# Kernel tuning notes

Hardware: AMD Instinct MI355X
Metric: run time of the kernel (lower is better)

## Reference

```python
import jax, jax.numpy as jnp
import numpy as np

NUM, B, C, H, W = 2, 8, 512, 32, 32


def setup_inputs() -> dict:
    key = jax.random.key(0)
    ks = jax.random.split(key, 6)
    s = 0.02  # weight init scale
    return {
        "feat_sources": jax.random.normal(ks[0], (NUM, B, C, H, W), jnp.float32),
        "feat_targets": jax.random.normal(ks[1], (NUM, B, C, H, W), jnp.float32),
        # 1x1 conv == per-pixel channel matmul: weight [num, C_out, C_in], bias [num, C]
        "Wq": jax.random.normal(ks[2], (NUM, C, C), jnp.float32) * s,
        "bq": jnp.zeros((NUM, C), jnp.float32),
        "Wk": jax.random.normal(ks[3], (NUM, C, C), jnp.float32) * s,
        "bk": jnp.zeros((NUM, C), jnp.float32),
        "Wv": jax.random.normal(ks[4], (NUM, C, C), jnp.float32) * s,
        "bv": jnp.zeros((NUM, C), jnp.float32),
    }


def reference(feat_sources, feat_targets, Wq, bq, Wk, bk, Wv, bv):
    num, Bt, Ct, Ht, Wt = feat_targets.shape
    HW = Ht * Wt
    tgt = feat_targets.reshape(num, Bt, Ct, HW)  # queries/values come from targets
    src = feat_sources.reshape(num, Bt, Ct, HW)  # keys come from sources

    # 1x1 conv projections (batched over the `num` heads of convs)
    Q = jnp.einsum('ioc,ibcn->ibno', Wq, tgt) + bq[:, None, None, :]   # (num, B, HW, C)
    K = jnp.einsum('joc,jbcn->jbon', Wk, src) + bk[:, None, :, None]   # (num, B, C, HW)
    V = jnp.einsum('ioc,ibcn->ibon', Wv, tgt) + bv[:, None, :, None]   # (num, B, C, HW)

    # energy[i, j] = bmm(pro_query_i, pro_key_j) over all target/source pairs
    energy = jnp.einsum('ibnc,jbcm->ijbnm', Q, K)                      # (num, num, B, HW, HW)

    # alpha: softmax over sources j of the scalar mean energy per (i, j)
    means = energy.mean(axis=(2, 3, 4))                                # (num, num)
    alphas = jax.nn.softmax(means, axis=1)

    # per-source softmax over keys, then summed across sources (torch.stack(...).sum(0))
    attn = jax.nn.softmax(energy, axis=-1).sum(axis=1)                 # (num, B, HW, HW)

    # out[b, c, n] = sum_m V[b, c, m] * attn[b, n, m]  (bmm(value, attention^T))
    out = jnp.einsum('ibcm,ibnm->ibcn', V, attn).reshape(num, Bt, Ct, Ht, Wt)
    return out, alphas
```

## Files before the change

### kernel.cpp

```cpp
#include <hip/hip_runtime.h>

#define NUMH 2
#define BATCH 8
#define CCH 512
#define HWN 1024

typedef unsigned short u16;
typedef unsigned int u32;
typedef _Float16 f16;
typedef __attribute__((ext_vector_type(8))) _Float16 f16x8;
typedef __attribute__((ext_vector_type(8))) short bf16x8;
typedef __attribute__((ext_vector_type(4))) float f32x4;

__device__ __forceinline__ u16 f2h(float x) {
    union { f16 h; u16 u; } cv;
    cv.h = (f16)x;
    return cv.u;
}
__device__ __forceinline__ u16 f2bf(float x) {
    u32 u = __float_as_uint(x);
    return (u16)((u + 0x7fffu + ((u >> 16) & 1u)) >> 16);
}
__device__ __forceinline__ float bf2f(u16 h) { return __uint_as_float(((u32)h) << 16); }

__device__ __forceinline__ float waveReduceSum(float v) {
#pragma unroll
    for (int off = 32; off > 0; off >>= 1) v += __shfl_xor(v, off);
    return v;
}

__global__ void zero_means_kernel(float* means) {
    if (threadIdx.x < 4) means[threadIdx.x] = 0.0f;
}
__global__ void zero_rs_kernel(float* rs, int n) {
    const int i = blockIdx.x * 256 + threadIdx.x;
    if (i < n) rs[i] = 0.0f;
}

__device__ __forceinline__ void stage_tile(const u16* __restrict__ src, int ld, int k0,
                                           u16* lds_arr, int w, int l) {
#pragma unroll
    for (int inst = 0; inst < 2; inst++) {
        const int p = w * 128 + inst * 64 + l;
        const int n = p >> 2;
        const int k4 = (p & 3) ^ ((n >> 1) & 3);
        const u16* g = src + n * ld + k0 + k4 * 8;
        u16* lp = lds_arr + (w * 128 + inst * 64) * 8;
        __builtin_amdgcn_global_load_lds(
            (const __attribute__((address_space(1))) u32*)g,
            (__attribute__((address_space(3))) u32*)lp, 16, 0, 0);
    }
}

template<bool BF>
__device__ __forceinline__ void mfma_block(const u16* sA, const u16* sB,
                                           int wr, int wc, int fr, int kq, f32x4 acc[4][4]) {
#define SLOT(row) (((row) * 4 + ((kq) ^ (((row) >> 1) & 3))) * 8)
    if constexpr (BF) {
        bf16x8 a[4], b[4];
#pragma unroll
        for (int mi = 0; mi < 4; mi++) a[mi] = *(const bf16x8*)(sA + SLOT(wr * 64 + mi * 16 + fr));
#pragma unroll
        for (int ni = 0; ni < 4; ni++) b[ni] = *(const bf16x8*)(sB + SLOT(wc * 64 + ni * 16 + fr));
#pragma unroll
        for (int mi = 0; mi < 4; mi++)
#pragma unroll
            for (int ni = 0; ni < 4; ni++)
                acc[mi][ni] = __builtin_amdgcn_mfma_f32_16x16x32_bf16(a[mi], b[ni], acc[mi][ni], 0, 0, 0);
    } else {
        f16x8 a[4], b[4];
#pragma unroll
        for (int mi = 0; mi < 4; mi++) a[mi] = *(const f16x8*)(sA + SLOT(wr * 64 + mi * 16 + fr));
#pragma unroll
        for (int ni = 0; ni < 4; ni++) b[ni] = *(const f16x8*)(sB + SLOT(wc * 64 + ni * 16 + fr));
#pragma unroll
        for (int mi = 0; mi < 4; mi++)
#pragma unroll
            for (int ni = 0; ni < 4; ni++)
                acc[mi][ni] = __builtin_amdgcn_mfma_f32_16x16x32_f16(a[mi], b[ni], acc[mi][ni], 0, 0, 0);
    }
#undef SLOT
}

template<bool BF>
__device__ __forceinline__ void mm_core(const u16* __restrict__ A, const u16* __restrict__ B,
                                        int K, int ldA, int ldB, u16* s, f32x4 acc[4][4]) {
    const int t = threadIdx.x, w = t >> 6, l = t & 63;
    const int wr = w >> 1, wc = w & 1, fr = l & 15, kq = l >> 4;
    u16 *sA0 = s, *sA1 = s + 4096, *sB0 = s + 8192, *sB1 = s + 12288;
    for (int k0 = 0; k0 < K; k0 += 64) {
        __syncthreads();
        stage_tile(A, ldA, k0, sA0, w, l);
        stage_tile(A, ldA, k0 + 32, sA1, w, l);
        stage_tile(B, ldB, k0, sB0, w, l);
        stage_tile(B, ldB, k0 + 32, sB1, w, l);
        __syncthreads();
        mfma_block<BF>(sA0, sB0, wr, wc, fr, kq, acc);
        mfma_block<BF>(sA1, sB1, wr, wc, fr, kq, acc);
    }
}

#define ACC_INIT(acc)                                         \
    f32x4 acc[4][4];                                          \
    _Pragma("unroll") for (int mi_ = 0; mi_ < 4; mi_++)       \
    _Pragma("unroll") for (int ni_ = 0; ni_ < 4; ni_++)       \
        acc[mi_][ni_] = (f32x4){0.f, 0.f, 0.f, 0.f};

#define SMEM_BYTES 33792

template<bool BF, bool BCOL, bool BROW>
__device__ __forceinline__ void epi_h16(char* smem, const f32x4 acc[4][4],
                                        const float* biasCol, const float* biasRow,
                                        u16* O, int ldO) {
    const int t = threadIdx.x, w = t >> 6, l = t & 63;
    const int wr = w >> 1, wc = w & 1, fr = l & 15, fq = l >> 4;
    u16* sb16 = (u16*)smem;
    u32* sb32 = (u32*)smem;
    __syncthreads();
#pragma unroll
    for (int ni = 0; ni < 4; ni++) {
        const int col = wc * 64 + ni * 16 + fr;
        const float bc = BCOL ? biasCol[col] : 0.0f;
#pragma unroll
        for (int mi = 0; mi < 4; mi++)
#pragma unroll
            for (int r = 0; r < 4; r++) {
                const int row = wr * 64 + mi * 16 + fq * 4 + r;
                const float v = acc[mi][ni][r] + bc + (BROW ? biasRow[row] : 0.0f);
                sb16[row * 132 + col] = BF ? f2bf(v) : f2h(v);
            }
    }
    __syncthreads();
#pragma unroll
    for (int it = 0; it < 8; it++) {
        const int idx = it * 256 + t;
        const int rr = idx >> 4, ch = idx & 15;
        const uint4 v4 = *(const uint4*)&sb32[rr * 66 + ch * 4];
        *(uint4*)&O[(size_t)rr * ldO + ch * 8] = v4;
    }
}

template<bool SCALE>
__device__ __forceinline__ void epi_f32(char* smem, const f32x4 acc[4][4],
                                        const float* ls, float* O, int ldO) {
    const int t = threadIdx.x, w = t >> 6, l = t & 63;
    const int wr = w >> 1, wc = w & 1, fr = l & 15, fq = l >> 4;
    float* sf = (float*)smem;
#pragma unroll
    for (int half = 0; half < 2; half++) {
        __syncthreads();
        if (wr == half) {
#pragma unroll
            for (int ni = 0; ni < 4; ni++) {
                const int col = wc * 64 + ni * 16 + fr;
                const float inv = SCALE ? 1.0f / ls[col] : 1.0f;
#pragma unroll
                for (int mi = 0; mi < 4; mi++)
#pragma unroll
                    for (int r = 0; r < 4; r++) {
                        const int rl = mi * 16 + fq * 4 + r;
                        sf[rl * 132 + col] = acc[mi][ni][r] * inv;
                    }
            }
        }
        __syncthreads();
#pragma unroll
        for (int it = 0; it < 8; it++) {
            const int idx = it * 256 + t;
            const int rr = idx >> 5, ch = idx & 31;
            const float4 v4 = *(const float4*)&sf[rr * 132 + ch * 4];
            *(float4*)&O[(size_t)(half * 64 + rr) * ldO + ch * 4] = v4;
        }
    }
}

__global__ __launch_bounds__(256) void tconv_kernel(
    const float* __restrict__ tgt, const float* __restrict__ src,
    u16* __restrict__ Tt, u16* __restrict__ St) {
    __shared__ float s[64][65];
    const int z = blockIdx.z;
    const int ib = z & 15;
    const float* X = (z >> 4 ? src : tgt) + (size_t)ib * CCH * HWN;
    u16* O = (z >> 4 ? St : Tt) + (size_t)ib * HWN * CCH;
    const int n0 = blockIdx.x * 64, c0 = blockIdx.y * 64;
    const int t = threadIdx.x;
    {
        const int cc = t >> 4, nch = (t & 15) * 4;
#pragma unroll
        for (int r = 0; r < 4; r++) {
            const float4 v = *(const float4*)&X[(size_t)(c0 + cc + r * 16) * HWN + n0 + nch];
            s[cc + r * 16][nch + 0] = v.x;
            s[cc + r * 16][nch + 1] = v.y;
            s[cc + r * 16][nch + 2] = v.z;
            s[cc + r * 16][nch + 3] = v.w;
        }
    }
    __syncthreads();
    const int nl = t >> 2;
    const int cb = (t & 3) * 16;
    __attribute__((aligned(16))) u16 hbuf[16];
#pragma unroll
    for (int cc = 0; cc < 16; cc++) hbuf[cc] = f2h(s[cb + cc][nl]);
    const size_t orow = (size_t)(n0 + nl) * CCH + c0 + cb;
    *(uint4*)&O[orow + 0] = *(const uint4*)&hbuf[0];
    *(uint4*)&O[orow + 8] = *(const uint4*)&hbuf[8];
}

__global__ __launch_bounds__(256) void convw_kernel(
    const float* __restrict__ Wq, const float* __restrict__ Wk, const float* __restrict__ Wv,
    u16* __restrict__ Wqh, u16* __restrict__ Wkh, u16* __restrict__ Wvh) {
    const int idx = (blockIdx.x * 256 + threadIdx.x) * 4;
    {
        const float4 v = *(const float4*)&Wq[idx];
        uint2 h = {(u32)f2h(v.x) | ((u32)f2h(v.y) << 16), (u32)f2h(v.z) | ((u32)f2h(v.w) << 16)};
        *(uint2*)&Wqh[idx] = h;
    }
    {
        const float4 v = *(const float4*)&Wk[idx];
        uint2 h = {(u32)f2h(v.x) | ((u32)f2h(v.y) << 16), (u32)f2h(v.z) | ((u32)f2h(v.w) << 16)};
        *(uint2*)&Wkh[idx] = h;
    }
    {
        const float4 v = *(const float4*)&Wv[idx];
        uint2 h = {(u32)f2h(v.x) | ((u32)f2h(v.y) << 16), (u32)f2h(v.z) | ((u32)f2h(v.w) << 16)};
        *(uint2*)&Wvh[idx] = h;
    }
}

__global__ __launch_bounds__(256) void proj_qk_kernel(
    const u16* __restrict__ Tt, const u16* __restrict__ St,
    const u16* __restrict__ Wqh, const u16* __restrict__ Wkh,
    const float* __restrict__ bq, const float* __restrict__ bk,
    u16* __restrict__ Qp, u16* __restrict__ Kp) {
    __shared__ __align__(16) char smem[SMEM_BYTES];
    const int z = blockIdx.z;
    const int b = z & 7, i = (z >> 3) & 1, p = z >> 4;
    const size_t ib = (size_t)(i * BATCH + b) * HWN * CCH;
    const u16* A = (p ? St : Tt) + ib;
    const u16* B = (p ? Wkh : Wqh) + (size_t)i * CCH * CCH;
    const float* bias = (p ? bk : bq) + i * CCH;
    u16* O = (p ? Kp : Qp) + ib;
    const int tile_m = blockIdx.y * 128, tile_n = blockIdx.x * 128;

    ACC_INIT(acc)
    mm_core<false>(A + (size_t)tile_m * CCH, B + (size_t)tile_n * CCH,
                   CCH, CCH, CCH, (u16*)smem, acc);

    epi_h16<false, true, false>(smem, acc, bias + tile_n, nullptr,
                                O + (size_t)tile_m * CCH + tile_n, CCH);
}

__global__ __launch_bounds__(256) void proj_v_kernel(
    const u16* __restrict__ Wvh, const u16* __restrict__ Tt,
    const float* __restrict__ bvv, u16* __restrict__ Vb) {
    __shared__ __align__(16) char smem[SMEM_BYTES];
    const int z = blockIdx.z;
    const int b = z & 7, i = z >> 3;
    const size_t ib = (size_t)(i * BATCH + b) * HWN * CCH;
    const u16* A = Wvh + (size_t)i * CCH * CCH;
    const u16* B = Tt + ib;
    const int tile_m = blockIdx.y * 128, tile_n = blockIdx.x * 128;

    ACC_INIT(acc)
    mm_core<false>(A + (size_t)tile_m * CCH, B + (size_t)tile_n * CCH,
                   CCH, CCH, CCH, (u16*)smem, acc);

    u16* Ov = Vb + (size_t)(i * BATCH + b) * CCH * HWN;
    epi_h16<true, false, true>(smem, acc, nullptr, bvv + i * CCH + tile_m,
                               Ov + (size_t)tile_m * HWN + tile_n, HWN);
}

__global__ __launch_bounds__(256) void gemmE_kernel(
    const u16* __restrict__ Qp, const u16* __restrict__ Kp,
    u16* __restrict__ P, float* __restrict__ rs, float* __restrict__ means,
    int b0, int Bc) {
    __shared__ __align__(16) char smem[SMEM_BYTES];
    __shared__ float redsum[4];
    const int z = blockIdx.z;
    const int j = z & 1, ib2 = z >> 1;
    const int i = ib2 / Bc, bb = ib2 % Bc, b = b0 + bb;
    const size_t offA = (size_t)(i * BATCH + b) * HWN * CCH;
    const size_t offB = (size_t)(j * BATCH + b) * HWN * CCH;
    const int tile_m = blockIdx.y * 128, tile_n = blockIdx.x * 128;
    u16* Po = P + (size_t)(ib2 * 2 + j) * HWN * HWN + (size_t)tile_m * HWN + tile_n;
    float* rsp = rs + (size_t)(ib2 * 2 + j) * HWN;

    ACC_INIT(acc)
    mm_core<false>(Qp + offA + (size_t)tile_m * CCH, Kp + offB + (size_t)tile_n * CCH,
                   CCH, CCH, CCH, (u16*)smem, acc);

    const int t = threadIdx.x, w = t >> 6, l = t & 63;
    const int wr = w >> 1, wc = w & 1, fr = l & 15, fq = l >> 4;
    u16* sb16 = (u16*)smem;
    u32* sb32 = (u32*)smem;
    __syncthreads();
    float tsum = 0.0f;
    float rowacc[4][4];
#pragma unroll
    for (int mi = 0; mi < 4; mi++)
#pragma unroll
        for (int r = 0; r < 4; r++) rowacc[mi][r] = 0.0f;
#pragma unroll
    for (int ni = 0; ni < 4; ni++) {
        const int col = wc * 64 + ni * 16 + fr;
#pragma unroll
        for (int mi = 0; mi < 4; mi++)
#pragma unroll
            for (int r = 0; r < 4; r++) {
                const int row = wr * 64 + mi * 16 + fq * 4 + r;
                const float raw = acc[mi][ni][r];
                tsum += raw;
                const u16 eb = f2bf(__expf(raw));
                rowacc[mi][r] += bf2f(eb);
                sb16[row * 132 + col] = eb;
            }
    }
    tsum = waveReduceSum(tsum);
    if (l == 0) redsum[w] = tsum;
#pragma unroll
    for (int mi = 0; mi < 4; mi++)
#pragma unroll
        for (int r = 0; r < 4; r++) {
            float v = rowacc[mi][r];
            v += __shfl_xor(v, 1); v += __shfl_xor(v, 2);
            v += __shfl_xor(v, 4); v += __shfl_xor(v, 8);
            if (fr == 0) atomicAdd(&rsp[tile_m + wr * 64 + mi * 16 + fq * 4 + r], v);
        }
    __syncthreads();
    if (t == 0) atomicAdd(&means[i * 2 + j], redsum[0] + redsum[1] + redsum[2] + redsum[3]);
#pragma unroll
    for (int it = 0; it < 8; it++) {
        const int idx = it * 256 + t;
        const int rr = idx >> 4, ch = idx & 15;
        const uint4 v4 = *(const uint4*)&sb32[rr * 66 + ch * 4];
        *(uint4*)&Po[(size_t)rr * HWN + ch * 8] = v4;
    }
}

__global__ __launch_bounds__(256) void gemmOut_kernel(
    const u16* __restrict__ Vb, const u16* __restrict__ P, const float* __restrict__ rs,
    float* __restrict__ outp, int b0, int Bc) {
    __shared__ __align__(16) char smem[SMEM_BYTES];
    const int ib2 = blockIdx.z;
    const int i = ib2 / Bc, bb = ib2 % Bc, b = b0 + bb;
    const u16* A = Vb + (size_t)(i * BATCH + b) * CCH * HWN;
    const u16* P0 = P + (size_t)(ib2 * 2 + 0) * HWN * HWN;
    const u16* P1 = P + (size_t)(ib2 * 2 + 1) * HWN * HWN;
    const float* rs0 = rs + (size_t)(ib2 * 2 + 0) * HWN;
    const float* rs1 = rs + (size_t)(ib2 * 2 + 1) * HWN;
    float* O = outp + (size_t)(i * BATCH + b) * CCH * HWN;
    const int tile_m = blockIdx.y * 128, tile_n = blockIdx.x * 128;
    const int t = threadIdx.x, w = t >> 6, l = t & 63;
    const int wc = w & 1, fr = l & 15;

    ACC_INIT(acc)
    mm_core<true>(A + (size_t)tile_m * HWN, P0 + (size_t)tile_n * HWN,
                  HWN, HWN, HWN, (u16*)smem, acc);
#pragma unroll
    for (int ni = 0; ni < 4; ni++) {
        const int col = tile_n + wc * 64 + ni * 16 + fr;
        const float sc = rs1[col] / rs0[col];
#pragma unroll
        for (int mi = 0; mi < 4; mi++) acc[mi][ni] *= sc;
    }
    mm_core<true>(A + (size_t)tile_m * HWN, P1 + (size_t)tile_n * HWN,
                  HWN, HWN, HWN, (u16*)smem, acc);

    epi_f32<true>(smem, acc, rs1 + tile_n, O + (size_t)tile_m * HWN + tile_n, HWN);
}

__global__ void alphas_kernel(const float* __restrict__ means, float* __restrict__ outp) {
    if (threadIdx.x != 0) return;
    const float cnt = (float)BATCH * (float)HWN * (float)HWN;
    float m[4];
#pragma unroll
    for (int k = 0; k < 4; k++) m[k] = means[k] / cnt;
#pragma unroll
    for (int i = 0; i < 2; i++) {
        const float a = m[i * 2 + 0], bsc = m[i * 2 + 1];
        const float mx = fmaxf(a, bsc);
        const float ea = __expf(a - mx), eb = __expf(bsc - mx);
        const float inv = 1.0f / (ea + eb);
        outp[i * 2 + 0] = ea * inv;
        outp[i * 2 + 1] = eb * inv;
    }
}

extern "C" void kernel_launch(void* const* d_in, const int* in_sizes, int n_in,
                              void* d_out, int out_size, void* d_ws, size_t ws_size,
                              hipStream_t stream) {
    const float* fsrc = (const float*)d_in[0];
    const float* ftgt = (const float*)d_in[1];
    const float* Wq = (const float*)d_in[2];
    const float* bq = (const float*)d_in[3];
    const float* Wk = (const float*)d_in[4];
    const float* bk = (const float*)d_in[5];
    const float* Wv = (const float*)d_in[6];
    const float* bv = (const float*)d_in[7];
    float* outp = (float*)d_out;

    const size_t SZ_ACT = (size_t)NUMH * BATCH * HWN * CCH * 2;
    const size_t SZ_W = (size_t)NUMH * CCH * CCH * 2;
    char* w = (char*)d_ws;
    u16* Qp = (u16*)w; w += SZ_ACT;
    u16* Kp = (u16*)w; w += SZ_ACT;
    u16* Vb = (u16*)w; w += SZ_ACT;
    u16* Wqh = (u16*)w; w += SZ_W;
    u16* Wkh = (u16*)w; w += SZ_W;
    u16* Wvh = (u16*)w; w += SZ_W;
    float* means = (float*)w; w += 64;
    float* rs = (float*)w; w += (size_t)NUMH * BATCH * 2 * HWN * 4;
    char* region = w;
    u16* Tt = (u16*)region;
    u16* St = (u16*)(region + SZ_ACT);

    const size_t base_used = (size_t)(region - (char*)d_ws);
    int Bc = 8;
    while (Bc > 1) {
        size_t need = (size_t)NUMH * Bc * 2 * HWN * HWN * 2;
        size_t tneed = need > 2 * SZ_ACT ? need : 2 * SZ_ACT;
        if (base_used + tneed <= ws_size) break;
        Bc >>= 1;
    }
    u16* P = (u16*)region;
    const int nrs = NUMH * Bc * 2 * HWN;

    zero_means_kernel<<<1, 64, 0, stream>>>(means);
    convw_kernel<<<512, 256, 0, stream>>>(Wq, Wk, Wv, Wqh, Wkh, Wvh);
    tconv_kernel<<<dim3(16, 8, 32), 256, 0, stream>>>(ftgt, fsrc, Tt, St);
    proj_qk_kernel<<<dim3(4, 8, 32), 256, 0, stream>>>(Tt, St, Wqh, Wkh, bq, bk, Qp, Kp);
    proj_v_kernel<<<dim3(8, 4, 16), 256, 0, stream>>>(Wvh, Tt, bv, Vb);

    const int nch = BATCH / Bc;
    for (int ch = 0; ch < nch; ch++) {
        const int b0 = ch * Bc;
        zero_rs_kernel<<<(nrs + 255) / 256, 256, 0, stream>>>(rs, nrs);
        gemmE_kernel<<<dim3(8, 8, NUMH * Bc * 2), 256, 0, stream>>>(Qp, Kp, P, rs, means, b0, Bc);
        gemmOut_kernel<<<dim3(8, 4, NUMH * Bc), 256, 0, stream>>>(Vb, P, rs, outp, b0, Bc);
    }
    alphas_kernel<<<1, 1, 0, stream>>>(means, outp + (out_size - 4));
}
```

Baseline: 201.0 us.

## Swizzle workgroup order across XCDs and shrink epilogue LDS staging

Adds a workgroup-ID remap that groups consecutive tiles onto the same XCD so they share L2, and applies it to all GEMM kernels. Epilogues are split into halves or quarters so the LDS staging buffer drops to 32 KB, which could raise occupancy. The energy epilogue now sums the unrounded exp values instead of the bf16-rounded ones, which slightly changes the normaliser against the stored probabilities. The extra halving passes add barriers per tile.

Measured after the change: 211.2 us. 5.1% more time.

```diff
diff --git a/kernel.cpp b/kernel.cpp
--- a/kernel.cpp
+++ b/kernel.cpp
@@ -21,12 +21,21 @@
     u32 u = __float_as_uint(x);
     return (u16)((u + 0x7fffu + ((u >> 16) & 1u)) >> 16);
 }
-__device__ __forceinline__ float bf2f(u16 h) { return __uint_as_float(((u32)h) << 16); }
 
 __device__ __forceinline__ float waveReduceSum(float v) {
 #pragma unroll
     for (int off = 32; off > 0; off >>= 1) v += __shfl_xor(v, off);
     return v;
+}
+
+__device__ __forceinline__ void swz_decode(int& x, int& y, int& z) {
+    const int gx = gridDim.x, gy = gridDim.y;
+    const int nwg = gx * gy * gridDim.z;
+    const int fid = blockIdx.x + gx * (blockIdx.y + gy * blockIdx.z);
+    const int cpx = nwg >> 3;
+    int swz = (fid & 7) * cpx + (fid >> 3);
+    x = swz % gx; swz /= gx;
+    y = swz % gy; z = swz / gy;
 }
 
 __global__ void zero_means_kernel(float* means) {
@@ -106,7 +115,7 @@
     _Pragma("unroll") for (int ni_ = 0; ni_ < 4; ni_++)       \
         acc[mi_][ni_] = (f32x4){0.f, 0.f, 0.f, 0.f};
 
-#define SMEM_BYTES 33792
+#define SMEM_BYTES 32768
 
 template<bool BF, bool BCOL, bool BROW>
 __device__ __forceinline__ void epi_h16(char* smem, const f32x4 acc[4][4],
@@ -116,27 +125,33 @@
     const int wr = w >> 1, wc = w & 1, fr = l & 15, fq = l >> 4;
     u16* sb16 = (u16*)smem;
     u32* sb32 = (u32*)smem;
-    __syncthreads();
-#pragma unroll
-    for (int ni = 0; ni < 4; ni++) {
-        const int col = wc * 64 + ni * 16 + fr;
-        const float bc = BCOL ? biasCol[col] : 0.0f;
-#pragma unroll
-        for (int mi = 0; mi < 4; mi++)
-#pragma unroll
-            for (int r = 0; r < 4; r++) {
-                const int row = wr * 64 + mi * 16 + fq * 4 + r;
-                const float v = acc[mi][ni][r] + bc + (BROW ? biasRow[row] : 0.0f);
-                sb16[row * 132 + col] = BF ? f2bf(v) : f2h(v);
+#pragma unroll
+    for (int half = 0; half < 2; half++) {
+        __syncthreads();
+        if (wr == half) {
+#pragma unroll
+            for (int ni = 0; ni < 4; ni++) {
+                const int col = wc * 64 + ni * 16 + fr;
+                const float bc = BCOL ? biasCol[col] : 0.0f;
+#pragma unroll
+                for (int mi = 0; mi < 4; mi++)
+#pragma unroll
+                    for (int r = 0; r < 4; r++) {
+                        const int lrow = mi * 16 + fq * 4 + r;
+                        const float v = acc[mi][ni][r] + bc +
+                                        (BROW ? biasRow[half * 64 + lrow] : 0.0f);
+                        sb16[lrow * 132 + col] = BF ? f2bf(v) : f2h(v);
+                    }
             }
-    }
-    __syncthreads();
-#pragma unroll
-    for (int it = 0; it < 8; it++) {
-        const int idx = it * 256 + t;
-        const int rr = idx >> 4, ch = idx & 15;
-        const uint4 v4 = *(const uint4*)&sb32[rr * 66 + ch * 4];
-        *(uint4*)&O[(size_t)rr * ldO + ch * 8] = v4;
+        }
+        __syncthreads();
+#pragma unroll
+        for (int it = 0; it < 4; it++) {
+            const int idx = it * 256 + t;
+            const int rr = idx >> 4, ch = idx & 15;
+            const uint4 v4 = *(const uint4*)&sb32[rr * 66 + ch * 4];
+            *(uint4*)&O[(size_t)(half * 64 + rr) * ldO + ch * 8] = v4;
+        }
     }
 }
 
@@ -147,29 +162,30 @@
     const int wr = w >> 1, wc = w & 1, fr = l & 15, fq = l >> 4;
     float* sf = (float*)smem;
 #pragma unroll
-    for (int half = 0; half < 2; half++) {
-        __syncthreads();
-        if (wr == half) {
+    for (int q = 0; q < 4; q++) {
+        __syncthreads();
+        if (wr == (q >> 1)) {
+            const int mi0 = (q & 1) * 2;
 #pragma unroll
             for (int ni = 0; ni < 4; ni++) {
                 const int col = wc * 64 + ni * 16 + fr;
                 const float inv = SCALE ? 1.0f / ls[col] : 1.0f;
 #pragma unroll
-                for (int mi = 0; mi < 4; mi++)
+                for (int mm = 0; mm < 2; mm++)
 #pragma unroll
                     for (int r = 0; r < 4; r++) {
-                        const int rl = mi * 16 + fq * 4 + r;
-                        sf[rl * 132 + col] = acc[mi][ni][r] * inv;
+                        const int lrow = mm * 16 + fq * 4 + r;
+                        sf[lrow * 132 + col] = acc[mi0 + mm][ni][r] * inv;
                     }
             }
         }
         __syncthreads();
 #pragma unroll
-        for (int it = 0; it < 8; it++) {
+        for (int it = 0; it < 4; it++) {
             const int idx = it * 256 + t;
             const int rr = idx >> 5, ch = idx & 31;
             const float4 v4 = *(const float4*)&sf[rr * 132 + ch * 4];
-            *(float4*)&O[(size_t)(half * 64 + rr) * ldO + ch * 4] = v4;
+            *(float4*)&O[(size_t)(q * 32 + rr) * ldO + ch * 4] = v4;
         }
     }
 }
@@ -233,14 +249,15 @@
     const float* __restrict__ bq, const float* __restrict__ bk,
     u16* __restrict__ Qp, u16* __restrict__ Kp) {
     __shared__ __align__(16) char smem[SMEM_BYTES];
-    const int z = blockIdx.z;
+    int bx, by, z;
+    swz_decode(bx, by, z);
     const int b = z & 7, i = (z >> 3) & 1, p = z >> 4;
     const size_t ib = (size_t)(i * BATCH + b) * HWN * CCH;
     const u16* A = (p ? St : Tt) + ib;
     const u16* B = (p ? Wkh : Wqh) + (size_t)i * CCH * CCH;
     const float* bias = (p ? bk : bq) + i * CCH;
     u16* O = (p ? Kp : Qp) + ib;
-    const int tile_m = blockIdx.y * 128, tile_n = blockIdx.x * 128;
+    const int tile_m = by * 128, tile_n = bx * 128;
 
     ACC_INIT(acc)
     mm_core<false>(A + (size_t)tile_m * CCH, B + (size_t)tile_n * CCH,
@@ -254,12 +271,13 @@
     const u16* __restrict__ Wvh, const u16* __restrict__ Tt,
     const float* __restrict__ bvv, u16* __restrict__ Vb) {
     __shared__ __align__(16) char smem[SMEM_BYTES];
-    const int z = blockIdx.z;
+    int bx, by, z;
+    swz_decode(bx, by, z);
     const int b = z & 7, i = z >> 3;
     const size_t ib = (size_t)(i * BATCH + b) * HWN * CCH;
     const u16* A = Wvh + (size_t)i * CCH * CCH;
     const u16* B = Tt + ib;
-    const int tile_m = blockIdx.y * 128, tile_n = blockIdx.x * 128;
+    const int tile_m = by * 128, tile_n = bx * 128;
 
     ACC_INIT(acc)
     mm_core<false>(A + (size_t)tile_m * CCH, B + (size_t)tile_n * CCH,
@@ -275,13 +293,13 @@
     u16* __restrict__ P, float* __restrict__ rs, float* __restrict__ means,
     int b0, int Bc) {
     __shared__ __align__(16) char smem[SMEM_BYTES];
-    __shared__ float redsum[4];
-    const int z = blockIdx.z;
+    int bx, by, z;
+    swz_decode(bx, by, z);
     const int j = z & 1, ib2 = z >> 1;
     const int i = ib2 / Bc, bb = ib2 % Bc, b = b0 + bb;
     const size_t offA = (size_t)(i * BATCH + b) * HWN * CCH;
     const size_t offB = (size_t)(j * BATCH + b) * HWN * CCH;
-    const int tile_m = blockIdx.y * 128, tile_n = blockIdx.x * 128;
+    const int tile_m = by * 128, tile_n = bx * 128;
     u16* Po = P + (size_t)(ib2 * 2 + j) * HWN * HWN + (size_t)tile_m * HWN + tile_n;
     float* rsp = rs + (size_t)(ib2 * 2 + j) * HWN;
 
@@ -293,7 +311,7 @@
     const int wr = w >> 1, wc = w & 1, fr = l & 15, fq = l >> 4;
     u16* sb16 = (u16*)smem;
     u32* sb32 = (u32*)smem;
-    __syncthreads();
+    float* redsum = (float*)(smem + 17408);
     float tsum = 0.0f;
     float rowacc[4][4];
 #pragma unroll
@@ -301,19 +319,33 @@
 #pragma unroll
         for (int r = 0; r < 4; r++) rowacc[mi][r] = 0.0f;
 #pragma unroll
-    for (int ni = 0; ni < 4; ni++) {
-        const int col = wc * 64 + ni * 16 + fr;
-#pragma unroll
-        for (int mi = 0; mi < 4; mi++)
-#pragma unroll
-            for (int r = 0; r < 4; r++) {
-                const int row = wr * 64 + mi * 16 + fq * 4 + r;
-                const float raw = acc[mi][ni][r];
-                tsum += raw;
-                const u16 eb = f2bf(__expf(raw));
-                rowacc[mi][r] += bf2f(eb);
-                sb16[row * 132 + col] = eb;
+    for (int half = 0; half < 2; half++) {
+        __syncthreads();
+        if (wr == half) {
+#pragma unroll
+            for (int ni = 0; ni < 4; ni++) {
+                const int col = wc * 64 + ni * 16 + fr;
+#pragma unroll
+                for (int mi = 0; mi < 4; mi++)
+#pragma unroll
+                    for (int r = 0; r < 4; r++) {
+                        const int lrow = mi * 16 + fq * 4 + r;
+                        const float raw = acc[mi][ni][r];
+                        tsum += raw;
+                        const float ex = __expf(raw);
+                        rowacc[mi][r] += ex;
+                        sb16[lrow * 132 + col] = f2bf(ex);
+                    }
             }
+        }
+        __syncthreads();
+#pragma unroll
+        for (int it = 0; it < 4; it++) {
+            const int idx = it * 256 + t;
+            const int rr = idx >> 4, ch = idx & 15;
+            const uint4 v4 = *(const uint4*)&sb32[rr * 66 + ch * 4];
+            *(uint4*)&Po[(size_t)(half * 64 + rr) * HWN + ch * 8] = v4;
+        }
     }
     tsum = waveReduceSum(tsum);
     if (l == 0) redsum[w] = tsum;
@@ -328,20 +360,14 @@
         }
     __syncthreads();
     if (t == 0) atomicAdd(&means[i * 2 + j], redsum[0] + redsum[1] + redsum[2] + redsum[3]);
-#pragma unroll
-    for (int it = 0; it < 8; it++) {
-        const int idx = it * 256 + t;
-        const int rr = idx >> 4, ch = idx & 15;
-        const uint4 v4 = *(const uint4*)&sb32[rr * 66 + ch * 4];
-        *(uint4*)&Po[(size_t)rr * HWN + ch * 8] = v4;
-    }
 }
 
 __global__ __launch_bounds__(256) void gemmOut_kernel(
     const u16* __restrict__ Vb, const u16* __restrict__ P, const float* __restrict__ rs,
     float* __restrict__ outp, int b0, int Bc) {
     __shared__ __align__(16) char smem[SMEM_BYTES];
-    const int ib2 = blockIdx.z;
+    int bx, by, ib2;
+    swz_decode(bx, by, ib2);
     const int i = ib2 / Bc, bb = ib2 % Bc, b = b0 + bb;
     const u16* A = Vb + (size_t)(i * BATCH + b) * CCH * HWN;
     const u16* P0 = P + (size_t)(ib2 * 2 + 0) * HWN * HWN;
@@ -349,7 +375,7 @@
     const float* rs0 = rs + (size_t)(ib2 * 2 + 0) * HWN;
     const float* rs1 = rs + (size_t)(ib2 * 2 + 1) * HWN;
     float* O = outp + (size_t)(i * BATCH + b) * CCH * HWN;
-    const int tile_m = blockIdx.y * 128, tile_n = blockIdx.x * 128;
+    const int tile_m = by * 128, tile_n = bx * 128;
     const int t = threadIdx.x, w = t >> 6, l = t & 63;
     const int wc = w & 1, fr = l & 15;
 
```
